# Kernel optimization log

Hardware: AMD Instinct MI355X
Metric: run time of the kernel (lower is better)

## Reference

```python
import jax, jax.numpy as jnp
import numpy as np

H_HEADS = 8

def _conv1x1(x, w):
    # x: (b, C_in, H, W), w: (C_out, C_in, 1, 1)
    return jax.lax.conv_general_dilated(
        x, w, window_strides=(1, 1), padding='VALID',
        dimension_numbers=('NCHW', 'OIHW', 'NCHW'))

def setup_inputs() -> dict:
    key = jax.random.key(0)
    kx, kq, kk, kv = jax.random.split(key, 4)
    x = jax.random.normal(kx, (16, 256, 64, 64), dtype=jnp.float32)
    sc = 1.0 / np.sqrt(256.0)
    wq = jax.random.normal(kq, (256, 256, 1, 1), dtype=jnp.float32) * sc
    wk = jax.random.normal(kk, (256, 256, 1, 1), dtype=jnp.float32) * sc
    wv = jax.random.normal(kv, (256, 256, 1, 1), dtype=jnp.float32) * sc
    return {"x": x, "wq": wq, "wk": wk, "wv": wv}

def reference(x, wq, wk, wv):
    b, _, Hs, Ws = x.shape
    h = H_HEADS
    v = _conv1x1(x, wv)                      # (b, C, H, W)
    C = v.shape[1]
    d = C // h
    q = _conv1x1(x, wq).reshape(b, h, d, -1)  # (b, h, d, N)
    k = _conv1x1(x, wk).reshape(b, h, d, -1)
    vflat = v.reshape(b, h, d, -1)
    # channel-attention: contract over spatial N -> (b, h, d, d)
    scores = jnp.einsum('bhdn,bhen->bhde', q, k) / jnp.sqrt(jnp.float32(h))
    attn_weights = jax.nn.softmax(scores, axis=-1)
    attn = jnp.einsum('bhde,bhen->bhdn', attn_weights, vflat)  # (b, h, d, N)
    # ChannelShuffle(groups=h): (b, h, d, H, W) -> (b, d, h, H, W) -> (b, C, H, W)
    shuffled = attn.reshape(b, h, d, Hs, Ws).transpose(0, 2, 1, 3, 4).reshape(b, C, Hs, Ws)
    out = shuffled + v
    return (out, attn_weights)
```

## Files before the change

### kernel.cpp

```cpp
#include <hip/hip_runtime.h>
#include <hip/hip_bf16.h>
#include <stdint.h>

typedef __attribute__((ext_vector_type(4))) float f32x4;
typedef __attribute__((ext_vector_type(8))) short bf16x8;
typedef __attribute__((ext_vector_type(4))) short bf16x4;
typedef __attribute__((ext_vector_type(4))) unsigned int u32x4;

__device__ __forceinline__ unsigned short f2bf_rne(float f) {
  union { float f; unsigned int u; } v; v.f = f;
  unsigned int r = v.u + 0x7FFFu + ((v.u >> 16) & 1u);
  return (unsigned short)(r >> 16);
}
__device__ __forceinline__ float bf2f(unsigned short s) {
  union { float f; unsigned int u; } v; v.u = ((unsigned int)s) << 16;
  return v.f;
}

__global__ __launch_bounds__(1024) void k_gram(const float* __restrict__ x,
                                               float* __restrict__ Gpart) {
  __shared__ __align__(16) unsigned char lds[256 * 128];
  const int b = blockIdx.y;
  const int n0 = blockIdx.x << 8;
  const int t = threadIdx.x;
  const int lane = t & 63;
  const int w = t >> 6;
  const int wm = (w >> 2) << 6;
  const int wn = (w & 3) << 6;
  const int c_ld = t >> 2;
  const int noct = t & 3;
  const int lrow = lane & 15;
  const int lkg = lane >> 4;

  f32x4 acc[4][4];
#pragma unroll
  for (int i = 0; i < 4; i++)
#pragma unroll
    for (int j = 0; j < 4; j++) acc[i][j] = (f32x4){0.f, 0.f, 0.f, 0.f};

  const float* gx = x + (((size_t)(b * 256 + c_ld)) << 12) + n0 + (noct << 3);
  f32x4 v0 = *(const f32x4*)(gx);
  f32x4 v1 = *(const f32x4*)(gx + 4);

  for (int sub = 0; sub < 8; sub++) {
    float vv[8] = {v0[0], v0[1], v0[2], v0[3], v1[0], v1[1], v1[2], v1[3]};
    unsigned short hi[8], lo[8];
#pragma unroll
    for (int j = 0; j < 8; j++) {
      hi[j] = f2bf_rne(vv[j]);
      lo[j] = f2bf_rne(vv[j] - bf2f(hi[j]));
    }
    u32x4 hw = {(unsigned)hi[0] | ((unsigned)hi[1] << 16),
                (unsigned)hi[2] | ((unsigned)hi[3] << 16),
                (unsigned)hi[4] | ((unsigned)hi[5] << 16),
                (unsigned)hi[6] | ((unsigned)hi[7] << 16)};
    u32x4 lw = {(unsigned)lo[0] | ((unsigned)lo[1] << 16),
                (unsigned)lo[2] | ((unsigned)lo[3] << 16),
                (unsigned)lo[4] | ((unsigned)lo[5] << 16),
                (unsigned)lo[6] | ((unsigned)lo[7] << 16)};

    __syncthreads();
    const int swz = (c_ld & 7) << 4;
    *(u32x4*)(lds + c_ld * 128 + (((noct << 4)) ^ swz)) = hw;
    *(u32x4*)(lds + c_ld * 128 + ((64 + (noct << 4)) ^ swz)) = lw;
    __syncthreads();

    if (sub < 7) {
      v0 = *(const f32x4*)(gx + ((sub + 1) << 5));
      v1 = *(const f32x4*)(gx + ((sub + 1) << 5) + 4);
    }

    bf16x8 bh[4], bl[4];
#pragma unroll
    for (int nf = 0; nf < 4; nf++) {
      int col = wn + (nf << 4) + lrow;
      int cs = (col & 7) << 4;
      bh[nf] = *(const bf16x8*)(lds + col * 128 + (((lkg << 4)) ^ cs));
      bl[nf] = *(const bf16x8*)(lds + col * 128 + ((64 + (lkg << 4)) ^ cs));
    }
#pragma unroll
    for (int mf = 0; mf < 4; mf++) {
      int row = wm + (mf << 4) + lrow;
      int rs = (row & 7) << 4;
      bf16x8 ah = *(const bf16x8*)(lds + row * 128 + (((lkg << 4)) ^ rs));
      bf16x8 al = *(const bf16x8*)(lds + row * 128 + ((64 + (lkg << 4)) ^ rs));
#pragma unroll
      for (int nf = 0; nf < 4; nf++) {
        acc[mf][nf] = __builtin_amdgcn_mfma_f32_16x16x32_bf16(ah, bh[nf], acc[mf][nf], 0, 0, 0);
        acc[mf][nf] = __builtin_amdgcn_mfma_f32_16x16x32_bf16(ah, bl[nf], acc[mf][nf], 0, 0, 0);
        acc[mf][nf] = __builtin_amdgcn_mfma_f32_16x16x32_bf16(al, bh[nf], acc[mf][nf], 0, 0, 0);
      }
    }
  }

  float* Gp = Gpart + (((size_t)(blockIdx.x * 16 + b)) << 16);
#pragma unroll
  for (int mf = 0; mf < 4; mf++)
#pragma unroll
    for (int nf = 0; nf < 4; nf++) {
      int col = wn + (nf << 4) + lrow;
#pragma unroll
      for (int r = 0; r < 4; r++) {
        int row = wm + (mf << 4) + (lkg << 2) + r;
        Gp[row * 256 + col] = acc[mf][nf][r];
      }
    }
}

__global__ __launch_bounds__(256) void k_reduce(const float* __restrict__ Gpart,
                                                float* __restrict__ G) {
  const size_t i = ((((size_t)blockIdx.x << 8) + threadIdx.x) << 2);
  f32x4 s = *(const f32x4*)(Gpart + i);
#pragma unroll
  for (int ch = 1; ch < 16; ch++)
    s += *(const f32x4*)(Gpart + (((size_t)ch) << 20) + i);
  *(f32x4*)(G + i) = s;
}

__global__ __launch_bounds__(512) void k_scores(const float* __restrict__ wq,
                                                const float* __restrict__ wk,
                                                const float* __restrict__ wv,
                                                const float* __restrict__ G,
                                                float* __restrict__ attn,
                                                unsigned short* __restrict__ Wout) {
  __shared__ float part[8][16][256];
  const int h = blockIdx.x, b = blockIdx.y, dg = blockIdx.z;
  const int t = threadIdx.x, lane = t & 63, w = t >> 6;

  float wqp[8];
  const float* wqb = wq + (size_t)(h * 32 + dg * 16) * 256 + w * 32;
#pragma unroll
  for (int r = 0; r < 8; r++)
    wqp[r] = wqb[(2 * r + (lane >> 5)) * 256 + (lane & 31)];

  f32x4 tp[16];
#pragma unroll
  for (int d = 0; d < 16; d++) tp[d] = (f32x4){0.f, 0.f, 0.f, 0.f};

  const float* Gb = G + ((size_t)b << 16) + (size_t)(w * 32) * 256 + (lane << 2);
  for (int s = 0; s < 32; s++) {
    f32x4 g = *(const f32x4*)(Gb + s * 256);
#pragma unroll
    for (int d = 0; d < 16; d++) {
      float wval = __shfl(wqp[d >> 1], ((d & 1) << 5) | s);
      tp[d] += g * wval;
    }
  }
#pragma unroll
  for (int d = 0; d < 16; d++)
    *(f32x4*)&part[w][d][lane << 2] = tp[d];
  __syncthreads();

#pragma unroll
  for (int u = 0; u < 2; u++) {
    int o = t * 2 + u;
    int d = o >> 6, q = (o & 63) << 2;
    f32x4 s = *(f32x4*)&part[0][d][q];
#pragma unroll
    for (int w2 = 1; w2 < 8; w2++) s += *(f32x4*)&part[w2][d][q];
    *(f32x4*)&part[0][d][q] = s;
  }
  __syncthreads();
  const float* Tb = &part[0][0][0];

  const int dls = t >> 5, es = t & 31;
  f32x4 sa = {0.f, 0.f, 0.f, 0.f};
  const float* Tr = Tb + dls * 256;
  const float* wkr = wk + (size_t)(h * 32 + es) * 256;
  for (int c4 = 0; c4 < 64; c4++)
    sa += *(const f32x4*)(Tr + (c4 << 2)) * *(const f32x4*)(wkr + (c4 << 2));
  float s = (sa[0] + sa[1] + sa[2] + sa[3]) * 0.35355339059327379f;

  float m = s;
#pragma unroll
  for (int off = 1; off < 32; off <<= 1) m = fmaxf(m, __shfl_xor(m, off));
  float p = expf(s - m);
  float su = p;
#pragma unroll
  for (int off = 1; off < 32; off <<= 1) su += __shfl_xor(su, off);
  float a = p / su;
  attn[(((b * 8 + h) * 32) + dg * 16 + dls) * 32 + es] = a;

  f32x4 o0 = {0.f, 0.f, 0.f, 0.f}, o1 = {0.f, 0.f, 0.f, 0.f};
  const float* wvh = wv + (size_t)(h * 32) * 256 + (lane << 2);
  for (int e = 0; e < 32; e++) {
    float a0 = __shfl(a, e);
    float a1 = __shfl(a, 32 + e);
    f32x4 vv = *(const f32x4*)(wvh + e * 256);
    o0 += vv * a0;
    o1 += vv * a1;
  }
  const int d0 = dg * 16 + 2 * w;
  const int co0 = d0 * 8 + h, co1 = (d0 + 1) * 8 + h;
  o0 += *(const f32x4*)(wv + (size_t)co0 * 256 + (lane << 2));
  o1 += *(const f32x4*)(wv + (size_t)co1 * 256 + (lane << 2));
  bf16x4 p0, p1;
#pragma unroll
  for (int j = 0; j < 4; j++) {
    p0[j] = (short)f2bf_rne(o0[j]);
    p1[j] = (short)f2bf_rne(o1[j]);
  }
  *(bf16x4*)(Wout + ((size_t)(b * 256 + co0) << 8) + (lane << 2)) = p0;
  *(bf16x4*)(Wout + ((size_t)(b * 256 + co1) << 8) + (lane << 2)) = p1;
}

__global__ __launch_bounds__(512) void k_out(const float* __restrict__ x,
                                             const unsigned short* __restrict__ Wout,
                                             float* __restrict__ out) {
  __shared__ __align__(16) unsigned short Bt[4096];
  const int b = blockIdx.y;
  const int nb = blockIdx.x << 7;
  const int t = threadIdx.x;
  const int lane = t & 63;
  const int w = t >> 6;
  const int wm = (w >> 1) << 6;
  const int wn = (w & 1) << 6;
  const int lrow = lane & 15;
  const int lkg = lane >> 4;

  f32x4 acc[4][4];
#pragma unroll
  for (int i = 0; i < 4; i++)
#pragma unroll
    for (int j = 0; j < 4; j++) acc[i][j] = (f32x4){0.f, 0.f, 0.f, 0.f};

  const int pos = lane >> 3;
  const int cblk = 2 * (pos & 3) + (pos >> 2);
  const int ctil = cblk * 4 + ((lane & 7) >> 1);
  const int noff = (lane & 1) << 3;
  const float* gxb = x + (((size_t)b) << 20) + (size_t)ctil * 4096 + nb + (w << 4) + noff;
  const unsigned int bt0 = (unsigned int)(uintptr_t)(&Bt[0]);

  f32x4 xa = *(const f32x4*)(gxb);
  f32x4 xb = *(const f32x4*)(gxb + 4);

  for (int kt = 0; kt < 8; kt++) {
    __syncthreads();
    bf16x8 pk;
#pragma unroll
    for (int j = 0; j < 4; j++) {
      pk[j] = (short)f2bf_rne(xa[j]);
      pk[4 + j] = (short)f2bf_rne(xb[j]);
    }
    *(bf16x8*)(Bt + (w << 9) + (lane << 3)) = pk;
    __syncthreads();

    if (kt < 7) {
      const float* nx = gxb + (((size_t)(kt + 1)) << 17);
      xa = *(const f32x4*)(nx);
      xb = *(const f32x4*)(nx + 4);
    }

    bf16x8 afr[4];
    const unsigned short* wrow = Wout + (((size_t)(b * 256)) << 8) + kt * 32 + (lkg << 3);
#pragma unroll
    for (int mf = 0; mf < 4; mf++) {
      int co = wm + (mf << 4) + lrow;
      afr[mf] = *(const bf16x8*)(wrow + ((size_t)co << 8));
    }

    bf16x4 t0[4], t1[4];
#pragma unroll
    for (int nf = 0; nf < 4; nf++) {
      unsigned int base = bt0 + (unsigned int)((((wn >> 4) + nf)) << 10) + (lane << 3);
      asm volatile("ds_read_b64_tr_b16 %0, %1" : "=v"(t0[nf]) : "v"(base) : "memory");
      asm volatile("ds_read_b64_tr_b16 %0, %1 offset:512" : "=v"(t1[nf]) : "v"(base) : "memory");
    }
    asm volatile("s_waitcnt lgkmcnt(0)" ::: "memory");
    __builtin_amdgcn_sched_barrier(0);

    bf16x8 bfr[4];
#pragma unroll
    for (int nf = 0; nf < 4; nf++) {
      bfr[nf][0] = t0[nf][0]; bfr[nf][1] = t0[nf][1];
      bfr[nf][2] = t0[nf][2]; bfr[nf][3] = t0[nf][3];
      bfr[nf][4] = t1[nf][0]; bfr[nf][5] = t1[nf][1];
      bfr[nf][6] = t1[nf][2]; bfr[nf][7] = t1[nf][3];
    }
#pragma unroll
    for (int mf = 0; mf < 4; mf++)
#pragma unroll
      for (int nf = 0; nf < 4; nf++)
        acc[mf][nf] = __builtin_amdgcn_mfma_f32_16x16x32_bf16(afr[mf], bfr[nf], acc[mf][nf], 0, 0, 0);
  }

  float* ob = out + (((size_t)b) << 20) + nb;
#pragma unroll
  for (int mf = 0; mf < 4; mf++)
#pragma unroll
    for (int nf = 0; nf < 4; nf++) {
      int col = wn + (nf << 4) + lrow;
#pragma unroll
      for (int r = 0; r < 4; r++) {
        int row = wm + (mf << 4) + (lkg << 2) + r;
        ob[((size_t)row << 12) + col] = acc[mf][nf][r];
      }
    }
}

extern "C" void kernel_launch(void* const* d_in, const int* in_sizes, int n_in,
                              void* d_out, int out_size, void* d_ws, size_t ws_size,
                              hipStream_t stream) {
  const float* x = (const float*)d_in[0];
  const float* wq = (const float*)d_in[1];
  const float* wk = (const float*)d_in[2];
  const float* wv = (const float*)d_in[3];
  float* out = (float*)d_out;
  float* attn = out + (size_t)16 * 256 * 4096;

  float* Gpart = out;

  char* ws = (char*)d_ws;
  float* G = (float*)ws;
  unsigned short* Wout = (unsigned short*)(ws + (4 << 20));

  k_gram<<<dim3(16, 16), dim3(1024), 0, stream>>>(x, Gpart);
  k_reduce<<<dim3(1024), dim3(256), 0, stream>>>(Gpart, G);
  k_scores<<<dim3(8, 16, 2), dim3(512), 0, stream>>>(wq, wk, wv, G, attn, Wout);
  k_out<<<dim3(32, 16), dim3(512), 0, stream>>>(x, Wout, out);
}
```

Before: 111.7 us.

## Exploit Gram symmetry: store upper tiles only and mirror in reduce

The Gram partial kernel now writes only the upper-triangular 64x64 warp tiles, assuming wm/wn are multiples of 64. The reduce kernel sums just the 10 upper tiles per batch and fills the lower half through an LDS transpose, so it reads and writes less partial-sum memory. The scores kernel replaces the register-plus-shuffle broadcast of wq with direct wave-uniform loads (readfirstlane) and fully unrolls the wv loop. The risk is correctness if the tile mapping does not line up with 64x64 blocks, plus lower parallelism from a 160-block reduce grid.

```diff
diff --git a/kernel.cpp b/kernel.cpp
--- a/kernel.cpp
+++ b/kernel.cpp
@@ -93,28 +93,62 @@
     }
   }
 
-  float* Gp = Gpart + (((size_t)(blockIdx.x * 16 + b)) << 16);
-#pragma unroll
-  for (int mf = 0; mf < 4; mf++)
-#pragma unroll
-    for (int nf = 0; nf < 4; nf++) {
-      int col = wn + (nf << 4) + lrow;
-#pragma unroll
-      for (int r = 0; r < 4; r++) {
-        int row = wm + (mf << 4) + (lkg << 2) + r;
-        Gp[row * 256 + col] = acc[mf][nf][r];
+  if (wm <= wn) {
+    float* Gp = Gpart + (((size_t)(blockIdx.x * 16 + b)) << 16);
+#pragma unroll
+    for (int mf = 0; mf < 4; mf++)
+#pragma unroll
+      for (int nf = 0; nf < 4; nf++) {
+        int col = wn + (nf << 4) + lrow;
+#pragma unroll
+        for (int r = 0; r < 4; r++) {
+          int row = wm + (mf << 4) + (lkg << 2) + r;
+          Gp[row * 256 + col] = acc[mf][nf][r];
+        }
       }
-    }
+  }
 }
 
 __global__ __launch_bounds__(256) void k_reduce(const float* __restrict__ Gpart,
                                                 float* __restrict__ G) {
-  const size_t i = ((((size_t)blockIdx.x << 8) + threadIdx.x) << 2);
-  f32x4 s = *(const f32x4*)(Gpart + i);
-#pragma unroll
-  for (int ch = 1; ch < 16; ch++)
-    s += *(const f32x4*)(Gpart + (((size_t)ch) << 20) + i);
-  *(f32x4*)(G + i) = s;
+  __shared__ float tl[64][68];
+  const int bx = blockIdx.x;
+  const int b = bx / 10;
+  int tp = bx % 10;
+  int i = 0;
+  while (tp >= 4 - i) { tp -= 4 - i; ++i; }
+  const int j = i + tp;
+  const int t = threadIdx.x;
+  const int r = t >> 2, cg = t & 3;
+
+  f32x4 s[4];
+#pragma unroll
+  for (int q = 0; q < 4; q++) s[q] = (f32x4){0.f, 0.f, 0.f, 0.f};
+  const float* src = Gpart + ((size_t)b << 16) + (size_t)(i * 64 + r) * 256 + j * 64 + cg * 16;
+  for (int ch = 0; ch < 16; ch++) {
+    const float* p = src + (((size_t)ch) << 20);
+#pragma unroll
+    for (int q = 0; q < 4; q++) s[q] += *(const f32x4*)(p + (q << 2));
+  }
+  float* dst = G + ((size_t)b << 16) + (size_t)(i * 64 + r) * 256 + j * 64 + cg * 16;
+#pragma unroll
+  for (int q = 0; q < 4; q++) *(f32x4*)(dst + (q << 2)) = s[q];
+
+  if (i != j) {
+#pragma unroll
+    for (int q = 0; q < 4; q++) *(f32x4*)&tl[r][cg * 16 + (q << 2)] = s[q];
+    __syncthreads();
+    const int c2 = t >> 2, g2 = t & 3;
+    float vals[16];
+#pragma unroll
+    for (int q = 0; q < 16; q++) vals[q] = tl[g2 * 16 + q][c2];
+    float* d2 = G + ((size_t)b << 16) + (size_t)(j * 64 + c2) * 256 + i * 64 + g2 * 16;
+#pragma unroll
+    for (int q = 0; q < 4; q++) {
+      f32x4 vv = {vals[4 * q], vals[4 * q + 1], vals[4 * q + 2], vals[4 * q + 3]};
+      *(f32x4*)(d2 + (q << 2)) = vv;
+    }
+  }
 }
 
 __global__ __launch_bounds__(512) void k_scores(const float* __restrict__ wq,
@@ -125,30 +159,24 @@
                                                 unsigned short* __restrict__ Wout) {
   __shared__ float part[8][16][256];
   const int h = blockIdx.x, b = blockIdx.y, dg = blockIdx.z;
-  const int t = threadIdx.x, lane = t & 63, w = t >> 6;
-
-  float wqp[8];
-  const float* wqb = wq + (size_t)(h * 32 + dg * 16) * 256 + w * 32;
-#pragma unroll
-  for (int r = 0; r < 8; r++)
-    wqp[r] = wqb[(2 * r + (lane >> 5)) * 256 + (lane & 31)];
-
+  const int t = threadIdx.x, lane = t & 63;
+  const int wu = __builtin_amdgcn_readfirstlane(t >> 6);
+
+  const float* wqrow = wq + (size_t)(h * 32 + dg * 16) * 256 + wu * 32;
   f32x4 tp[16];
 #pragma unroll
   for (int d = 0; d < 16; d++) tp[d] = (f32x4){0.f, 0.f, 0.f, 0.f};
 
-  const float* Gb = G + ((size_t)b << 16) + (size_t)(w * 32) * 256 + (lane << 2);
+  const float* Gb = G + ((size_t)b << 16) + (size_t)(wu * 32) * 256 + (lane << 2);
   for (int s = 0; s < 32; s++) {
     f32x4 g = *(const f32x4*)(Gb + s * 256);
 #pragma unroll
-    for (int d = 0; d < 16; d++) {
-      float wval = __shfl(wqp[d >> 1], ((d & 1) << 5) | s);
-      tp[d] += g * wval;
-    }
+    for (int d = 0; d < 16; d++)
+      tp[d] += g * wqrow[d * 256 + s];
   }
 #pragma unroll
   for (int d = 0; d < 16; d++)
-    *(f32x4*)&part[w][d][lane << 2] = tp[d];
+    *(f32x4*)&part[wu][d][lane << 2] = tp[d];
   __syncthreads();
 
 #pragma unroll
@@ -183,6 +211,7 @@
 
   f32x4 o0 = {0.f, 0.f, 0.f, 0.f}, o1 = {0.f, 0.f, 0.f, 0.f};
   const float* wvh = wv + (size_t)(h * 32) * 256 + (lane << 2);
+#pragma unroll
   for (int e = 0; e < 32; e++) {
     float a0 = __shfl(a, e);
     float a1 = __shfl(a, 32 + e);
@@ -190,7 +219,7 @@
     o0 += vv * a0;
     o1 += vv * a1;
   }
-  const int d0 = dg * 16 + 2 * w;
+  const int d0 = dg * 16 + 2 * wu;
   const int co0 = d0 * 8 + h, co1 = (d0 + 1) * 8 + h;
   o0 += *(const f32x4*)(wv + (size_t)co0 * 256 + (lane << 2));
   o1 += *(const f32x4*)(wv + (size_t)co1 * 256 + (lane << 2));
@@ -315,7 +344,7 @@
   unsigned short* Wout = (unsigned short*)(ws + (4 << 20));
 
   k_gram<<<dim3(16, 16), dim3(1024), 0, stream>>>(x, Gpart);
-  k_reduce<<<dim3(1024), dim3(256), 0, stream>>>(Gpart, G);
+  k_reduce<<<dim3(160), dim3(256), 0, stream>>>(Gpart, G);
   k_scores<<<dim3(8, 16, 2), dim3(512), 0, stream>>>(wq, wk, wv, G, attn, Wout);
   k_out<<<dim3(32, 16), dim3(512), 0, stream>>>(x, Wout, out);
 }
```

After: 103.8 us. -7.0%, faster.
